# Kernel optimization log

Measured on AMD Instinct MI355X. Metric: run time of the kernel, lower is better.

The kernel has to match this reference:

```python
import jax, jax.numpy as jnp
import numpy as np

N = 50000      # nodes
E = 800000     # edges (avg in-degree 16, first N are self-loops)
H = 8          # heads
D = 16         # per-head dim (out_dim in the torch module)
IN = 128       # in_dim (= H*D)
SCALE = float(np.sqrt(D))


def setup_inputs() -> dict:
    key = jax.random.key(0)
    ks = jax.random.split(key, 8)
    query = jax.random.normal(ks[0], (N, IN), jnp.float32)
    key_x = jax.random.normal(ks[1], (N, IN), jnp.float32)
    value = jax.random.normal(ks[2], (N, IN), jnp.float32)
    # nn.Linear weights [out_features, in_features], no bias (use_bias=False)
    w_std = 1.0 / np.sqrt(IN)
    WQ = jax.random.normal(ks[3], (H * D, IN), jnp.float32) * w_std
    WK = jax.random.normal(ks[4], (H * D, IN), jnp.float32) * w_std
    WV = jax.random.normal(ks[5], (H * D, IN), jnp.float32) * w_std
    # edges: self-loops for every node (guarantees in-degree >= 1) + random edges
    loops = jnp.arange(N, dtype=jnp.int32)
    rsrc = jax.random.randint(ks[6], (E - N,), 0, N, jnp.int32)
    rdst = jax.random.randint(ks[7], (E - N,), 0, N, jnp.int32)
    edge_src = jnp.concatenate([loops, rsrc])
    edge_dst = jnp.concatenate([loops, rdst])
    return {"query": query, "key": key_x, "value": value,
            "WQ": WQ, "WK": WK, "WV": WV,
            "edge_src": edge_src, "edge_dst": edge_dst}


def reference(query, key, value, WQ, WK, WV, edge_src, edge_dst):
    n = query.shape[0]
    Qh = (query @ WQ.T).reshape(n, H, D)   # [N,H,D]
    Kh = (key @ WK.T).reshape(n, H, D)
    Vh = (value @ WV.T).reshape(n, H, D)
    # per-edge score: sum over head dim of K[src] * Q[dst]  (src_dot_dst)
    s = jnp.einsum('ehd,ehd->eh', Kh[edge_src], Qh[edge_dst])  # [E,H]
    # scaled_exp: exp(clamp(score / sqrt(D), -5, 5))
    a = jnp.exp(jnp.clip(s / SCALE, -5.0, 5.0))                # [E,H]
    # scatter-sum weighted V and normalizer z to destination nodes
    wV = jax.ops.segment_sum(a[:, :, None] * Vh[edge_src], edge_dst, num_segments=n)  # [N,H,D]
    z = jax.ops.segment_sum(a, edge_dst, num_segments=n)                               # [N,H]
    return wV / z[:, :, None]
```

## Files before the change

kernel.cpp:

```cpp
#include <hip/hip_runtime.h>

#define HD  128
#define CAP 64

typedef short bf16x8 __attribute__((ext_vector_type(8)));
typedef float f32x4  __attribute__((ext_vector_type(4)));

static __device__ __forceinline__ unsigned short f2bf_bits(float f) {
    union { float f; unsigned u; } x; x.f = f;
    unsigned r = x.u + 0x7FFF + ((x.u >> 16) & 1);
    return (unsigned short)(r >> 16);
}
static __device__ __forceinline__ float bf2f(unsigned short s) {
    union { unsigned u; float f; } x; x.u = ((unsigned)s) << 16;
    return x.f;
}

__global__ __launch_bounds__(256) void k_scatcvt(
    const int* __restrict__ esrc, const int* __restrict__ edst,
    int* __restrict__ cursor, int* __restrict__ csr, int E, int nsb,
    const float* __restrict__ wq, const float* __restrict__ wk,
    const float* __restrict__ wv, short* __restrict__ wb)
{
    int bid = blockIdx.x;
    if (bid < nsb) {
        int i = bid * 256 + threadIdx.x;
        if (i < E) {
            int d = edst[i];
            int p = atomicAdd(&cursor[d], 1);
            if (p < CAP) csr[d * CAP + p] = esrc[i];
        }
        return;
    }
    int t = (bid - nsb) * 256 + threadIdx.x;
    if (t >= 3 * 16384 / 4) return;
    int flat = t * 4;
    int m = flat >> 14;
    int off = flat & 16383;
    const float* W = (m == 0) ? wq : (m == 1) ? wk : wv;
    float4 v = *(const float4*)(W + off);
    short4 s;
    s.x = (short)f2bf_bits(v.x);
    s.y = (short)f2bf_bits(v.y);
    s.z = (short)f2bf_bits(v.z);
    s.w = (short)f2bf_bits(v.w);
    *(short4*)(wb + flat) = s;
}

__global__ __launch_bounds__(256) void k_proj(
    const float* __restrict__ q, const float* __restrict__ k, const float* __restrict__ v,
    const short* __restrict__ wb,
    float* __restrict__ qh, short* __restrict__ kvb,
    int n, int ntiles)
{
    int pid = blockIdx.x;
    int m = pid / ntiles;
    int tile = pid - m * ntiles;
    const float* X = (m == 0) ? q : (m == 1) ? k : v;
    const short* W = wb + m * 16384;

    int wave = threadIdx.x >> 6, lane = threadIdx.x & 63;
    int lm = lane & 15, lg = lane >> 4;
    const short* wp = W + lm * HD + lg * 8;

    int row0 = tile * 64 + wave * 16;
    int arow = row0 + lm; if (arow >= n) arow = n - 1;
    const float* xp = X + (size_t)arow * HD + lg * 8;

    bf16x8 a[4];
    #pragma unroll
    for (int kk = 0; kk < 4; kk++) {
        float4 p0 = *(const float4*)(xp + kk * 32);
        float4 p1 = *(const float4*)(xp + kk * 32 + 4);
        bf16x8 t;
        t[0] = (short)f2bf_bits(p0.x); t[1] = (short)f2bf_bits(p0.y);
        t[2] = (short)f2bf_bits(p0.z); t[3] = (short)f2bf_bits(p0.w);
        t[4] = (short)f2bf_bits(p1.x); t[5] = (short)f2bf_bits(p1.y);
        t[6] = (short)f2bf_bits(p1.z); t[7] = (short)f2bf_bits(p1.w);
        a[kk] = t;
    }

    f32x4 acc[8];
    #pragma unroll
    for (int nt = 0; nt < 8; nt++) { f32x4 z = {0.f, 0.f, 0.f, 0.f}; acc[nt] = z; }

    #pragma unroll
    for (int nt = 0; nt < 8; nt++) {
        #pragma unroll
        for (int kk = 0; kk < 4; kk++) {
            bf16x8 b = *(const bf16x8*)(wp + nt * 16 * HD + kk * 32);
            acc[nt] = __builtin_amdgcn_mfma_f32_16x16x32_bf16(a[kk], b, acc[nt], 0, 0, 0);
        }
    }

    if (m == 0) {
        #pragma unroll
        for (int nt = 0; nt < 8; nt++)
            #pragma unroll
            for (int i = 0; i < 4; i++) {
                int r = row0 + lg * 4 + i;
                if (r < n) qh[(size_t)r * HD + nt * 16 + lm] = acc[nt][i];
            }
    } else {
        short* base = kvb + ((m == 1) ? 0 : HD);
        #pragma unroll
        for (int nt = 0; nt < 8; nt++)
            #pragma unroll
            for (int i = 0; i < 4; i++) {
                int r = row0 + lg * 4 + i;
                if (r < n) base[(size_t)r * 256 + nt * 16 + lm] =
                    (short)f2bf_bits(acc[nt][i]);
            }
    }
}

__global__ __launch_bounds__(256) void k_gather(
    const float* __restrict__ qh, const short* __restrict__ kvb,
    const int* __restrict__ cursor, const int* __restrict__ csr,
    float* __restrict__ out, int n)
{
    int wave = threadIdx.x >> 6;
    int lane = threadIdx.x & 63;
    int v = blockIdx.x * 4 + wave;
    if (v >= n) return;
    int j = lane & 31;

    float4 qv = *(const float4*)&qh[(size_t)v * HD + 4 * j];
    int beg = v * CAP;
    int cnt = cursor[v]; if (cnt > CAP) cnt = CAP;
    int end = beg + cnt;

    float4 acc = {0.f, 0.f, 0.f, 0.f};
    float z = 0.f;

    int e = beg;
    for (; e + 3 < end; e += 4) {
        int u0 = csr[e];
        int u1 = csr[e + 1];
        int u2 = csr[e + 2];
        int u3 = csr[e + 3];
        ushort4 kv0 = *(const ushort4*)&kvb[(size_t)u0 * 256 + 4 * lane];
        ushort4 kv1 = *(const ushort4*)&kvb[(size_t)u1 * 256 + 4 * lane];
        ushort4 kv2 = *(const ushort4*)&kvb[(size_t)u2 * 256 + 4 * lane];
        ushort4 kv3 = *(const ushort4*)&kvb[(size_t)u3 * 256 + 4 * lane];
        float x00 = bf2f(kv0.x), x01 = bf2f(kv0.y), x02 = bf2f(kv0.z), x03 = bf2f(kv0.w);
        float x10 = bf2f(kv1.x), x11 = bf2f(kv1.y), x12 = bf2f(kv1.z), x13 = bf2f(kv1.w);
        float x20 = bf2f(kv2.x), x21 = bf2f(kv2.y), x22 = bf2f(kv2.z), x23 = bf2f(kv2.w);
        float x30 = bf2f(kv3.x), x31 = bf2f(kv3.y), x32 = bf2f(kv3.z), x33 = bf2f(kv3.w);
        float p0 = x00 * qv.x + x01 * qv.y + x02 * qv.z + x03 * qv.w;
        float p1 = x10 * qv.x + x11 * qv.y + x12 * qv.z + x13 * qv.w;
        float p2 = x20 * qv.x + x21 * qv.y + x22 * qv.z + x23 * qv.w;
        float p3 = x30 * qv.x + x31 * qv.y + x32 * qv.z + x33 * qv.w;
        p0 += __shfl_xor(p0, 1); p1 += __shfl_xor(p1, 1);
        p2 += __shfl_xor(p2, 1); p3 += __shfl_xor(p3, 1);
        p0 += __shfl_xor(p0, 2); p1 += __shfl_xor(p1, 2);
        p2 += __shfl_xor(p2, 2); p3 += __shfl_xor(p3, 2);
        float a0 = __expf(fminf(fmaxf(p0 * 0.25f, -5.f), 5.f));
        float a1 = __expf(fminf(fmaxf(p1 * 0.25f, -5.f), 5.f));
        float a2 = __expf(fminf(fmaxf(p2 * 0.25f, -5.f), 5.f));
        float a3 = __expf(fminf(fmaxf(p3 * 0.25f, -5.f), 5.f));
        float av0 = __shfl_xor(a0, 32);
        float av1 = __shfl_xor(a1, 32);
        float av2 = __shfl_xor(a2, 32);
        float av3 = __shfl_xor(a3, 32);
        z += (a0 + a1) + (a2 + a3);
        acc.x += av0 * x00 + av1 * x10 + av2 * x20 + av3 * x30;
        acc.y += av0 * x01 + av1 * x11 + av2 * x21 + av3 * x31;
        acc.z += av0 * x02 + av1 * x12 + av2 * x22 + av3 * x32;
        acc.w += av0 * x03 + av1 * x13 + av2 * x23 + av3 * x33;
    }
    for (; e < end; ++e) {
        int u = csr[e];
        ushort4 kv = *(const ushort4*)&kvb[(size_t)u * 256 + 4 * lane];
        float x0 = bf2f(kv.x), x1 = bf2f(kv.y), x2 = bf2f(kv.z), x3 = bf2f(kv.w);
        float p = x0 * qv.x + x1 * qv.y + x2 * qv.z + x3 * qv.w;
        p += __shfl_xor(p, 1);
        p += __shfl_xor(p, 2);
        float a = __expf(fminf(fmaxf(p * 0.25f, -5.f), 5.f));
        float av = __shfl_xor(a, 32);
        z += a;
        acc.x += av * x0; acc.y += av * x1; acc.z += av * x2; acc.w += av * x3;
    }

    float zz = __shfl_xor(z, 32);
    if (lane >= 32) {
        float inv = 1.f / zz;
        float4 o = { acc.x * inv, acc.y * inv, acc.z * inv, acc.w * inv };
        *(float4*)&out[(size_t)v * HD + 4 * j] = o;
    }
}

extern "C" void kernel_launch(void* const* d_in, const int* in_sizes, int n_in,
                              void* d_out, int out_size, void* d_ws, size_t ws_size,
                              hipStream_t stream)
{
    const float* query = (const float*)d_in[0];
    const float* key   = (const float*)d_in[1];
    const float* value = (const float*)d_in[2];
    const float* WQ    = (const float*)d_in[3];
    const float* WK    = (const float*)d_in[4];
    const float* WV    = (const float*)d_in[5];
    const int*   esrc  = (const int*)d_in[6];
    const int*   edst  = (const int*)d_in[7];
    int n = in_sizes[0] / HD;
    int E = in_sizes[6];

    char* ws = (char*)d_ws;
    size_t off = 0;
    auto carve = [&](size_t bytes) -> void* {
        void* p = ws + off;
        off += (bytes + 255) & ~size_t(255);
        return p;
    };
    float* qh     = (float*)carve((size_t)n * HD * 4);
    short* kvb    = (short*)carve((size_t)n * 256 * 2);
    short* wb     = (short*)carve((size_t)3 * 16384 * 2);
    int*   cursor = (int*)carve((size_t)n * 4);
    int*   csr    = (int*)carve((size_t)n * CAP * 4);
    (void)ws_size;

    hipMemsetAsync(cursor, 0, (size_t)n * 4, stream);

    int nsb = (E + 255) / 256;
    k_scatcvt<<<nsb + 48, 256, 0, stream>>>(esrc, edst, cursor, csr, E, nsb,
                                            WQ, WK, WV, wb);

    int ntiles = (n + 63) / 64;
    k_proj<<<3 * ntiles, 256, 0, stream>>>(query, key, value, wb, qh, kvb, n, ntiles);

    k_gather<<<(n + 3) / 4, 256, 0, stream>>>(qh, kvb, cursor, csr,
                                              (float*)d_out, n);
}
```

Measured before the change: 168.2 us.

## Fuse edge scatter with projection, two row tiles per block, kernel zeroing

```diff
diff --git a/kernel.cpp b/kernel.cpp
--- a/kernel.cpp
+++ b/kernel.cpp
@@ -16,11 +16,36 @@
     return x.f;
 }
 
-__global__ __launch_bounds__(256) void k_scatcvt(
+__global__ __launch_bounds__(256) void k_pre(
+    const float* __restrict__ wq, const float* __restrict__ wk,
+    const float* __restrict__ wv, short* __restrict__ wb,
+    int* __restrict__ cursor, int n)
+{
+    int t = blockIdx.x * blockDim.x + threadIdx.x;
+    int nthr = gridDim.x * blockDim.x;
+    for (int i = t; i < 3 * 16384 / 4; i += nthr) {
+        int flat = i * 4;
+        int m = flat >> 14;
+        int off = flat & 16383;
+        const float* W = (m == 0) ? wq : (m == 1) ? wk : wv;
+        float4 v = *(const float4*)(W + off);
+        short4 s;
+        s.x = (short)f2bf_bits(v.x);
+        s.y = (short)f2bf_bits(v.y);
+        s.z = (short)f2bf_bits(v.z);
+        s.w = (short)f2bf_bits(v.w);
+        *(short4*)(wb + flat) = s;
+    }
+    for (int i = t; i < n; i += nthr) cursor[i] = 0;
+}
+
+__global__ __launch_bounds__(256) void k_spro(
     const int* __restrict__ esrc, const int* __restrict__ edst,
     int* __restrict__ cursor, int* __restrict__ csr, int E, int nsb,
-    const float* __restrict__ wq, const float* __restrict__ wk,
-    const float* __restrict__ wv, short* __restrict__ wb)
+    const float* __restrict__ q, const float* __restrict__ k, const float* __restrict__ v,
+    const short* __restrict__ wb,
+    float* __restrict__ qh, short* __restrict__ kvb,
+    int n, int npairs)
 {
     int bid = blockIdx.x;
     if (bid < nsb) {
@@ -32,30 +57,9 @@
         }
         return;
     }
-    int t = (bid - nsb) * 256 + threadIdx.x;
-    if (t >= 3 * 16384 / 4) return;
-    int flat = t * 4;
-    int m = flat >> 14;
-    int off = flat & 16383;
-    const float* W = (m == 0) ? wq : (m == 1) ? wk : wv;
-    float4 v = *(const float4*)(W + off);
-    short4 s;
-    s.x = (short)f2bf_bits(v.x);
-    s.y = (short)f2bf_bits(v.y);
-    s.z = (short)f2bf_bits(v.z);
-    s.w = (short)f2bf_bits(v.w);
-    *(short4*)(wb + flat) = s;
-}
-
-__global__ __launch_bounds__(256) void k_proj(
-    const float* __restrict__ q, const float* __restrict__ k, const float* __restrict__ v,
-    const short* __restrict__ wb,
-    float* __restrict__ qh, short* __restrict__ kvb,
-    int n, int ntiles)
-{
-    int pid = blockIdx.x;
-    int m = pid / ntiles;
-    int tile = pid - m * ntiles;
+    int pid = bid - nsb;
+    int m = pid / npairs;
+    int pr = pid - m * npairs;
     const float* X = (m == 0) ? q : (m == 1) ? k : v;
     const short* W = wb + m * 16384;
 
@@ -63,33 +67,51 @@
     int lm = lane & 15, lg = lane >> 4;
     const short* wp = W + lm * HD + lg * 8;
 
-    int row0 = tile * 64 + wave * 16;
-    int arow = row0 + lm; if (arow >= n) arow = n - 1;
-    const float* xp = X + (size_t)arow * HD + lg * 8;
-
-    bf16x8 a[4];
+    int rowA = pr * 128 + wave * 16;
+    int rowB = rowA + 64;
+    int arA = rowA + lm; if (arA >= n) arA = n - 1;
+    int arB = rowB + lm; if (arB >= n) arB = n - 1;
+    const float* xpA = X + (size_t)arA * HD + lg * 8;
+    const float* xpB = X + (size_t)arB * HD + lg * 8;
+
+    float4 pA[8], pB[8];
     #pragma unroll
     for (int kk = 0; kk < 4; kk++) {
-        float4 p0 = *(const float4*)(xp + kk * 32);
-        float4 p1 = *(const float4*)(xp + kk * 32 + 4);
-        bf16x8 t;
-        t[0] = (short)f2bf_bits(p0.x); t[1] = (short)f2bf_bits(p0.y);
-        t[2] = (short)f2bf_bits(p0.z); t[3] = (short)f2bf_bits(p0.w);
-        t[4] = (short)f2bf_bits(p1.x); t[5] = (short)f2bf_bits(p1.y);
-        t[6] = (short)f2bf_bits(p1.z); t[7] = (short)f2bf_bits(p1.w);
-        a[kk] = t;
-    }
-
-    f32x4 acc[8];
-    #pragma unroll
-    for (int nt = 0; nt < 8; nt++) { f32x4 z = {0.f, 0.f, 0.f, 0.f}; acc[nt] = z; }
+        pA[2 * kk]     = *(const float4*)(xpA + kk * 32);
+        pA[2 * kk + 1] = *(const float4*)(xpA + kk * 32 + 4);
+        pB[2 * kk]     = *(const float4*)(xpB + kk * 32);
+        pB[2 * kk + 1] = *(const float4*)(xpB + kk * 32 + 4);
+    }
+    bf16x8 a0[4], a1[4];
+    #pragma unroll
+    for (int kk = 0; kk < 4; kk++) {
+        bf16x8 t0, t1;
+        t0[0] = (short)f2bf_bits(pA[2*kk].x);   t0[1] = (short)f2bf_bits(pA[2*kk].y);
+        t0[2] = (short)f2bf_bits(pA[2*kk].z);   t0[3] = (short)f2bf_bits(pA[2*kk].w);
+        t0[4] = (short)f2bf_bits(pA[2*kk+1].x); t0[5] = (short)f2bf_bits(pA[2*kk+1].y);
+        t0[6] = (short)f2bf_bits(pA[2*kk+1].z); t0[7] = (short)f2bf_bits(pA[2*kk+1].w);
+        a0[kk] = t0;
+        t1[0] = (short)f2bf_bits(pB[2*kk].x);   t1[1] = (short)f2bf_bits(pB[2*kk].y);
+        t1[2] = (short)f2bf_bits(pB[2*kk].z);   t1[3] = (short)f2bf_bits(pB[2*kk].w);
+        t1[4] = (short)f2bf_bits(pB[2*kk+1].x); t1[5] = (short)f2bf_bits(pB[2*kk+1].y);
+        t1[6] = (short)f2bf_bits(pB[2*kk+1].z); t1[7] = (short)f2bf_bits(pB[2*kk+1].w);
+        a1[kk] = t1;
+    }
+
+    f32x4 acc0[8], acc1[8];
+    #pragma unroll
+    for (int nt = 0; nt < 8; nt++) {
+        f32x4 z = {0.f, 0.f, 0.f, 0.f};
+        acc0[nt] = z; acc1[nt] = z;
+    }
 
     #pragma unroll
     for (int nt = 0; nt < 8; nt++) {
         #pragma unroll
         for (int kk = 0; kk < 4; kk++) {
             bf16x8 b = *(const bf16x8*)(wp + nt * 16 * HD + kk * 32);
-            acc[nt] = __builtin_amdgcn_mfma_f32_16x16x32_bf16(a[kk], b, acc[nt], 0, 0, 0);
+            acc0[nt] = __builtin_amdgcn_mfma_f32_16x16x32_bf16(a0[kk], b, acc0[nt], 0, 0, 0);
+            acc1[nt] = __builtin_amdgcn_mfma_f32_16x16x32_bf16(a1[kk], b, acc1[nt], 0, 0, 0);
         }
     }
 
@@ -98,8 +120,10 @@
         for (int nt = 0; nt < 8; nt++)
             #pragma unroll
             for (int i = 0; i < 4; i++) {
-                int r = row0 + lg * 4 + i;
-                if (r < n) qh[(size_t)r * HD + nt * 16 + lm] = acc[nt][i];
+                int rA = rowA + lg * 4 + i;
+                int rB = rowB + lg * 4 + i;
+                if (rA < n) qh[(size_t)rA * HD + nt * 16 + lm] = acc0[nt][i];
+                if (rB < n) qh[(size_t)rB * HD + nt * 16 + lm] = acc1[nt][i];
             }
     } else {
         short* base = kvb + ((m == 1) ? 0 : HD);
@@ -107,9 +131,12 @@
         for (int nt = 0; nt < 8; nt++)
             #pragma unroll
             for (int i = 0; i < 4; i++) {
-                int r = row0 + lg * 4 + i;
-                if (r < n) base[(size_t)r * 256 + nt * 16 + lm] =
-                    (short)f2bf_bits(acc[nt][i]);
+                int rA = rowA + lg * 4 + i;
+                int rB = rowB + lg * 4 + i;
+                if (rA < n) base[(size_t)rA * 256 + nt * 16 + lm] =
+                    (short)f2bf_bits(acc0[nt][i]);
+                if (rB < n) base[(size_t)rB * 256 + nt * 16 + lm] =
+                    (short)f2bf_bits(acc1[nt][i]);
             }
     }
 }
@@ -219,14 +246,14 @@
     int*   csr    = (int*)carve((size_t)n * CAP * 4);
     (void)ws_size;
 
-    hipMemsetAsync(cursor, 0, (size_t)n * 4, stream);
+    k_pre<<<64, 256, 0, stream>>>(WQ, WK, WV, wb, cursor, n);
 
     int nsb = (E + 255) / 256;
-    k_scatcvt<<<nsb + 48, 256, 0, stream>>>(esrc, edst, cursor, csr, E, nsb,
-                                            WQ, WK, WV, wb);
-
     int ntiles = (n + 63) / 64;
-    k_proj<<<3 * ntiles, 256, 0, stream>>>(query, key, value, wb, qh, kvb, n, ntiles);
+    int npairs = (ntiles + 1) / 2;
+    k_spro<<<nsb + 3 * npairs, 256, 0, stream>>>(esrc, edst, cursor, csr, E, nsb,
+                                                 query, key, value, wb, qh, kvb,
+                                                 n, npairs);
 
     k_gather<<<(n + 3) / 4, 256, 0, stream>>>(qh, kvb, cursor, csr,
                                               (float*)d_out, n);
```

Result: no change. 165.8 us (-1.4%).

## Stage projection outputs through swizzled LDS and deepen gather unroll to eight

Applied to the files above, without the earlier changes.

```diff
diff --git a/kernel.cpp b/kernel.cpp
--- a/kernel.cpp
+++ b/kernel.cpp
@@ -16,35 +16,39 @@
     return x.f;
 }
 
-__global__ __launch_bounds__(256) void k_scatcvt(
+__global__ __launch_bounds__(256) void k_pre(
+    const float* __restrict__ wq, const float* __restrict__ wk,
+    const float* __restrict__ wv, short* __restrict__ wb,
+    int* __restrict__ cursor, int n)
+{
+    int t = blockIdx.x * blockDim.x + threadIdx.x;
+    int nthr = gridDim.x * blockDim.x;
+    for (int i = t; i < 3 * 16384 / 4; i += nthr) {
+        int flat = i * 4;
+        int m = flat >> 14;
+        int off = flat & 16383;
+        const float* W = (m == 0) ? wq : (m == 1) ? wk : wv;
+        float4 v = *(const float4*)(W + off);
+        short4 s;
+        s.x = (short)f2bf_bits(v.x);
+        s.y = (short)f2bf_bits(v.y);
+        s.z = (short)f2bf_bits(v.z);
+        s.w = (short)f2bf_bits(v.w);
+        *(short4*)(wb + flat) = s;
+    }
+    for (int i = t; i < n; i += nthr) cursor[i] = 0;
+}
+
+__global__ __launch_bounds__(256) void k_scat(
     const int* __restrict__ esrc, const int* __restrict__ edst,
-    int* __restrict__ cursor, int* __restrict__ csr, int E, int nsb,
-    const float* __restrict__ wq, const float* __restrict__ wk,
-    const float* __restrict__ wv, short* __restrict__ wb)
-{
-    int bid = blockIdx.x;
-    if (bid < nsb) {
-        int i = bid * 256 + threadIdx.x;
-        if (i < E) {
-            int d = edst[i];
-            int p = atomicAdd(&cursor[d], 1);
-            if (p < CAP) csr[d * CAP + p] = esrc[i];
-        }
-        return;
-    }
-    int t = (bid - nsb) * 256 + threadIdx.x;
-    if (t >= 3 * 16384 / 4) return;
-    int flat = t * 4;
-    int m = flat >> 14;
-    int off = flat & 16383;
-    const float* W = (m == 0) ? wq : (m == 1) ? wk : wv;
-    float4 v = *(const float4*)(W + off);
-    short4 s;
-    s.x = (short)f2bf_bits(v.x);
-    s.y = (short)f2bf_bits(v.y);
-    s.z = (short)f2bf_bits(v.z);
-    s.w = (short)f2bf_bits(v.w);
-    *(short4*)(wb + flat) = s;
+    int* __restrict__ cursor, int* __restrict__ csr, int E)
+{
+    int i = blockIdx.x * 256 + threadIdx.x;
+    if (i < E) {
+        int d = edst[i];
+        int p = atomicAdd(&cursor[d], 1);
+        if (p < CAP) csr[d * CAP + p] = esrc[i];
+    }
 }
 
 __global__ __launch_bounds__(256) void k_proj(
@@ -53,6 +57,7 @@
     float* __restrict__ qh, short* __restrict__ kvb,
     int n, int ntiles)
 {
+    __shared__ float smem[64 * 128];
     int pid = blockIdx.x;
     int m = pid / ntiles;
     int tile = pid - m * ntiles;
@@ -63,8 +68,9 @@
     int lm = lane & 15, lg = lane >> 4;
     const short* wp = W + lm * HD + lg * 8;
 
-    int row0 = tile * 64 + wave * 16;
-    int arow = row0 + lm; if (arow >= n) arow = n - 1;
+    int row0 = tile * 64;
+    int rw = row0 + wave * 16;
+    int arow = rw + lm; if (arow >= n) arow = n - 1;
     const float* xp = X + (size_t)arow * HD + lg * 8;
 
     bf16x8 a[4];
@@ -98,19 +104,49 @@
         for (int nt = 0; nt < 8; nt++)
             #pragma unroll
             for (int i = 0; i < 4; i++) {
-                int r = row0 + lg * 4 + i;
-                if (r < n) qh[(size_t)r * HD + nt * 16 + lm] = acc[nt][i];
-            }
+                int rl = wave * 16 + lg * 4 + i;
+                smem[rl * 128 + ((nt ^ (rl & 7)) * 16 + lm)] = acc[nt][i];
+            }
+        __syncthreads();
+        int t = threadIdx.x;
+        #pragma unroll
+        for (int p = 0; p < 4; p++) {
+            int flat = p * 256 + t;
+            int r = flat >> 4;
+            int c8 = (flat & 15) * 8;
+            int g = c8 >> 4, rem = c8 & 15;
+            const float* sp = &smem[r * 128 + ((g ^ (r & 7)) * 16 + rem)];
+            int rg = row0 + r;
+            if (rg < n) {
+                *(float4*)&qh[(size_t)rg * HD + c8]     = *(const float4*)sp;
+                *(float4*)&qh[(size_t)rg * HD + c8 + 4] = *(const float4*)(sp + 4);
+            }
+        }
     } else {
-        short* base = kvb + ((m == 1) ? 0 : HD);
+        short* sb = (short*)smem;
         #pragma unroll
         for (int nt = 0; nt < 8; nt++)
             #pragma unroll
             for (int i = 0; i < 4; i++) {
-                int r = row0 + lg * 4 + i;
-                if (r < n) base[(size_t)r * 256 + nt * 16 + lm] =
-                    (short)f2bf_bits(acc[nt][i]);
-            }
+                int rl = wave * 16 + lg * 4 + i;
+                sb[rl * 128 + ((nt ^ (rl & 7)) * 16 + lm)] = (short)f2bf_bits(acc[nt][i]);
+            }
+        __syncthreads();
+        int t = threadIdx.x;
+        int coff = (m == 1) ? 0 : HD;
+        #pragma unroll
+        for (int p = 0; p < 4; p++) {
+            int flat = p * 256 + t;
+            int r = flat >> 4;
+            int c8 = (flat & 15) * 8;
+            int g = c8 >> 4, rem = c8 & 15;
+            const short* sp = &sb[r * 128 + ((g ^ (r & 7)) * 16 + rem)];
+            int rg = row0 + r;
+            if (rg < n) {
+                *(short4*)&kvb[(size_t)rg * 256 + coff + c8]     = *(const short4*)sp;
+                *(short4*)&kvb[(size_t)rg * 256 + coff + c8 + 4] = *(const short4*)(sp + 4);
+            }
+        }
     }
 }
 
@@ -134,40 +170,60 @@
     float z = 0.f;
 
     int e = beg;
+    for (; e + 7 < end; e += 8) {
+        int u[8];
+        #pragma unroll
+        for (int q8 = 0; q8 < 8; q8++) u[q8] = csr[e + q8];
+        ushort4 kvx[8];
+        #pragma unroll
+        for (int q8 = 0; q8 < 8; q8++)
+            kvx[q8] = *(const ushort4*)&kvb[(size_t)u[q8] * 256 + 4 * lane];
+        float x0[8], x1[8], x2[8], x3[8], p[8];
+        #pragma unroll
+        for (int q8 = 0; q8 < 8; q8++) {
+            x0[q8] = bf2f(kvx[q8].x); x1[q8] = bf2f(kvx[q8].y);
+            x2[q8] = bf2f(kvx[q8].z); x3[q8] = bf2f(kvx[q8].w);
+            p[q8] = x0[q8] * qv.x + x1[q8] * qv.y + x2[q8] * qv.z + x3[q8] * qv.w;
+        }
+        #pragma unroll
+        for (int q8 = 0; q8 < 8; q8++) p[q8] += __shfl_xor(p[q8], 1);
+        #pragma unroll
+        for (int q8 = 0; q8 < 8; q8++) p[q8] += __shfl_xor(p[q8], 2);
+        float a[8], av[8];
+        #pragma unroll
+        for (int q8 = 0; q8 < 8; q8++)
+            a[q8] = __expf(fminf(fmaxf(p[q8] * 0.25f, -5.f), 5.f));
+        #pragma unroll
+        for (int q8 = 0; q8 < 8; q8++) av[q8] = __shfl_xor(a[q8], 32);
+        #pragma unroll
+        for (int q8 = 0; q8 < 8; q8++) {
+            z += a[q8];
+            acc.x += av[q8] * x0[q8];
+            acc.y += av[q8] * x1[q8];
+            acc.z += av[q8] * x2[q8];
+            acc.w += av[q8] * x3[q8];
+        }
+    }
     for (; e + 3 < end; e += 4) {
-        int u0 = csr[e];
-        int u1 = csr[e + 1];
-        int u2 = csr[e + 2];
-        int u3 = csr[e + 3];
-        ushort4 kv0 = *(const ushort4*)&kvb[(size_t)u0 * 256 + 4 * lane];
-        ushort4 kv1 = *(const ushort4*)&kvb[(size_t)u1 * 256 + 4 * lane];
-        ushort4 kv2 = *(const ushort4*)&kvb[(size_t)u2 * 256 + 4 * lane];
-        ushort4 kv3 = *(const ushort4*)&kvb[(size_t)u3 * 256 + 4 * lane];
-        float x00 = bf2f(kv0.x), x01 = bf2f(kv0.y), x02 = bf2f(kv0.z), x03 = bf2f(kv0.w);
-        float x10 = bf2f(kv1.x), x11 = bf2f(kv1.y), x12 = bf2f(kv1.z), x13 = bf2f(kv1.w);
-        float x20 = bf2f(kv2.x), x21 = bf2f(kv2.y), x22 = bf2f(kv2.z), x23 = bf2f(kv2.w);
-        float x30 = bf2f(kv3.x), x31 = bf2f(kv3.y), x32 = bf2f(kv3.z), x33 = bf2f(kv3.w);
-        float p0 = x00 * qv.x + x01 * qv.y + x02 * qv.z + x03 * qv.w;
-        float p1 = x10 * qv.x + x11 * qv.y + x12 * qv.z + x13 * qv.w;
-        float p2 = x20 * qv.x + x21 * qv.y + x22 * qv.z + x23 * qv.w;
-        float p3 = x30 * qv.x + x31 * qv.y + x32 * qv.z + x33 * qv.w;
-        p0 += __shfl_xor(p0, 1); p1 += __shfl_xor(p1, 1);
-        p2 += __shfl_xor(p2, 1); p3 += __shfl_xor(p3, 1);
-        p0 += __shfl_xor(p0, 2); p1 += __shfl_xor(p1, 2);
-        p2 += __shfl_xor(p2, 2); p3 += __shfl_xor(p3, 2);
-        float a0 = __expf(fminf(fmaxf(p0 * 0.25f, -5.f), 5.f));
-        float a1 = __expf(fminf(fmaxf(p1 * 0.25f, -5.f), 5.f));
-        float a2 = __expf(fminf(fmaxf(p2 * 0.25f, -5.f), 5.f));
-        float a3 = __expf(fminf(fmaxf(p3 * 0.25f, -5.f), 5.f));
-        float av0 = __shfl_xor(a0, 32);
-        float av1 = __shfl_xor(a1, 32);
-        float av2 = __shfl_xor(a2, 32);
-        float av3 = __shfl_xor(a3, 32);
-        z += (a0 + a1) + (a2 + a3);
-        acc.x += av0 * x00 + av1 * x10 + av2 * x20 + av3 * x30;
-        acc.y += av0 * x01 + av1 * x11 + av2 * x21 + av3 * x31;
-        acc.z += av0 * x02 + av1 * x12 + av2 * x22 + av3 * x32;
-        acc.w += av0 * x03 + av1 * x13 + av2 * x23 + av3 * x33;
+        int u[4];
+        #pragma unroll
+        for (int q4 = 0; q4 < 4; q4++) u[q4] = csr[e + q4];
+        ushort4 kvx[4];
+        #pragma unroll
+        for (int q4 = 0; q4 < 4; q4++)
+            kvx[q4] = *(const ushort4*)&kvb[(size_t)u[q4] * 256 + 4 * lane];
+        #pragma unroll
+        for (int q4 = 0; q4 < 4; q4++) {
+            float x0 = bf2f(kvx[q4].x), x1 = bf2f(kvx[q4].y);
+            float x2 = bf2f(kvx[q4].z), x3 = bf2f(kvx[q4].w);
+            float p = x0 * qv.x + x1 * qv.y + x2 * qv.z + x3 * qv.w;
+            p += __shfl_xor(p, 1);
+            p += __shfl_xor(p, 2);
+            float a = __expf(fminf(fmaxf(p * 0.25f, -5.f), 5.f));
+            float av = __shfl_xor(a, 32);
+            z += a;
+            acc.x += av * x0; acc.y += av * x1; acc.z += av * x2; acc.w += av * x3;
+        }
     }
     for (; e < end; ++e) {
         int u = csr[e];
@@ -219,11 +275,9 @@
     int*   csr    = (int*)carve((size_t)n * CAP * 4);
     (void)ws_size;
 
-    hipMemsetAsync(cursor, 0, (size_t)n * 4, stream);
-
-    int nsb = (E + 255) / 256;
-    k_scatcvt<<<nsb + 48, 256, 0, stream>>>(esrc, edst, cursor, csr, E, nsb,
-                                            WQ, WK, WV, wb);
+    k_pre<<<64, 256, 0, stream>>>(WQ, WK, WV, wb, cursor, n);
+
+    k_scat<<<(E + 255) / 256, 256, 0, stream>>>(esrc, edst, cursor, csr, E);
 
     int ntiles = (n + 63) / 64;
     k_proj<<<3 * ntiles, 256, 0, stream>>>(query, key, value, wb, qh, kvb, n, ntiles);
```

Result: slower. 179.0 us (+6.4%).

## Stage bf16 weights in swizzled LDS with persistent projection blocks

Applied to the files above, without the earlier changes.

```diff
diff --git a/kernel.cpp b/kernel.cpp
--- a/kernel.cpp
+++ b/kernel.cpp
@@ -16,35 +16,39 @@
     return x.f;
 }
 
-__global__ __launch_bounds__(256) void k_scatcvt(
+__global__ __launch_bounds__(256) void k_pre(
+    const float* __restrict__ wq, const float* __restrict__ wk,
+    const float* __restrict__ wv, short* __restrict__ wb,
+    int* __restrict__ cursor, int n)
+{
+    int t = blockIdx.x * blockDim.x + threadIdx.x;
+    int nthr = gridDim.x * blockDim.x;
+    for (int i = t; i < 3 * 16384 / 4; i += nthr) {
+        int flat = i * 4;
+        int m = flat >> 14;
+        int off = flat & 16383;
+        const float* W = (m == 0) ? wq : (m == 1) ? wk : wv;
+        float4 v = *(const float4*)(W + off);
+        short4 s;
+        s.x = (short)f2bf_bits(v.x);
+        s.y = (short)f2bf_bits(v.y);
+        s.z = (short)f2bf_bits(v.z);
+        s.w = (short)f2bf_bits(v.w);
+        *(short4*)(wb + flat) = s;
+    }
+    for (int i = t; i < n; i += nthr) cursor[i] = 0;
+}
+
+__global__ __launch_bounds__(256) void k_scat(
     const int* __restrict__ esrc, const int* __restrict__ edst,
-    int* __restrict__ cursor, int* __restrict__ csr, int E, int nsb,
-    const float* __restrict__ wq, const float* __restrict__ wk,
-    const float* __restrict__ wv, short* __restrict__ wb)
-{
-    int bid = blockIdx.x;
-    if (bid < nsb) {
-        int i = bid * 256 + threadIdx.x;
-        if (i < E) {
-            int d = edst[i];
-            int p = atomicAdd(&cursor[d], 1);
-            if (p < CAP) csr[d * CAP + p] = esrc[i];
-        }
-        return;
-    }
-    int t = (bid - nsb) * 256 + threadIdx.x;
-    if (t >= 3 * 16384 / 4) return;
-    int flat = t * 4;
-    int m = flat >> 14;
-    int off = flat & 16383;
-    const float* W = (m == 0) ? wq : (m == 1) ? wk : wv;
-    float4 v = *(const float4*)(W + off);
-    short4 s;
-    s.x = (short)f2bf_bits(v.x);
-    s.y = (short)f2bf_bits(v.y);
-    s.z = (short)f2bf_bits(v.z);
-    s.w = (short)f2bf_bits(v.w);
-    *(short4*)(wb + flat) = s;
+    int* __restrict__ cursor, int* __restrict__ csr, int E)
+{
+    int i = blockIdx.x * 256 + threadIdx.x;
+    if (i < E) {
+        int d = edst[i];
+        int p = atomicAdd(&cursor[d], 1);
+        if (p < CAP) csr[d * CAP + p] = esrc[i];
+    }
 }
 
 __global__ __launch_bounds__(256) void k_proj(
@@ -53,64 +57,79 @@
     float* __restrict__ qh, short* __restrict__ kvb,
     int n, int ntiles)
 {
-    int pid = blockIdx.x;
-    int m = pid / ntiles;
-    int tile = pid - m * ntiles;
+    __shared__ short wlds[16384];
+    int bid = blockIdx.x;
+    int m = bid % 3;
+    int t0 = bid / 3;
     const float* X = (m == 0) ? q : (m == 1) ? k : v;
     const short* W = wb + m * 16384;
 
-    int wave = threadIdx.x >> 6, lane = threadIdx.x & 63;
+    int tid = threadIdx.x;
+    for (int i = tid; i < 2048; i += 256) {
+        int row = i >> 4, g = i & 15;
+        *(bf16x8*)&wlds[row * 128 + ((g ^ (row & 15)) * 8)] =
+            *(const bf16x8*)&W[row * 128 + g * 8];
+    }
+    __syncthreads();
+
+    int wave = tid >> 6, lane = tid & 63;
     int lm = lane & 15, lg = lane >> 4;
-    const short* wp = W + lm * HD + lg * 8;
-
-    int row0 = tile * 64 + wave * 16;
-    int arow = row0 + lm; if (arow >= n) arow = n - 1;
-    const float* xp = X + (size_t)arow * HD + lg * 8;
-
-    bf16x8 a[4];
-    #pragma unroll
-    for (int kk = 0; kk < 4; kk++) {
-        float4 p0 = *(const float4*)(xp + kk * 32);
-        float4 p1 = *(const float4*)(xp + kk * 32 + 4);
-        bf16x8 t;
-        t[0] = (short)f2bf_bits(p0.x); t[1] = (short)f2bf_bits(p0.y);
-        t[2] = (short)f2bf_bits(p0.z); t[3] = (short)f2bf_bits(p0.w);
-        t[4] = (short)f2bf_bits(p1.x); t[5] = (short)f2bf_bits(p1.y);
-        t[6] = (short)f2bf_bits(p1.z); t[7] = (short)f2bf_bits(p1.w);
-        a[kk] = t;
-    }
-
-    f32x4 acc[8];
-    #pragma unroll
-    for (int nt = 0; nt < 8; nt++) { f32x4 z = {0.f, 0.f, 0.f, 0.f}; acc[nt] = z; }
-
-    #pragma unroll
-    for (int nt = 0; nt < 8; nt++) {
+
+    for (int tile = t0; tile < ntiles; tile += 256) {
+        int row0 = tile * 64 + wave * 16;
+        int arow = row0 + lm; if (arow >= n) arow = n - 1;
+        const float* xp = X + (size_t)arow * HD + lg * 8;
+
+        float4 p0[4], p1[4];
         #pragma unroll
         for (int kk = 0; kk < 4; kk++) {
-            bf16x8 b = *(const bf16x8*)(wp + nt * 16 * HD + kk * 32);
-            acc[nt] = __builtin_amdgcn_mfma_f32_16x16x32_bf16(a[kk], b, acc[nt], 0, 0, 0);
-        }
-    }
-
-    if (m == 0) {
-        #pragma unroll
-        for (int nt = 0; nt < 8; nt++)
+            p0[kk] = *(const float4*)(xp + kk * 32);
+            p1[kk] = *(const float4*)(xp + kk * 32 + 4);
+        }
+        bf16x8 a[4];
+        #pragma unroll
+        for (int kk = 0; kk < 4; kk++) {
+            bf16x8 t;
+            t[0] = (short)f2bf_bits(p0[kk].x); t[1] = (short)f2bf_bits(p0[kk].y);
+            t[2] = (short)f2bf_bits(p0[kk].z); t[3] = (short)f2bf_bits(p0[kk].w);
+            t[4] = (short)f2bf_bits(p1[kk].x); t[5] = (short)f2bf_bits(p1[kk].y);
+            t[6] = (short)f2bf_bits(p1[kk].z); t[7] = (short)f2bf_bits(p1[kk].w);
+            a[kk] = t;
+        }
+
+        f32x4 acc[8];
+        #pragma unroll
+        for (int nt = 0; nt < 8; nt++) { f32x4 z = {0.f, 0.f, 0.f, 0.f}; acc[nt] = z; }
+
+        #pragma unroll
+        for (int nt = 0; nt < 8; nt++) {
             #pragma unroll
-            for (int i = 0; i < 4; i++) {
-                int r = row0 + lg * 4 + i;
-                if (r < n) qh[(size_t)r * HD + nt * 16 + lm] = acc[nt][i];
+            for (int kk = 0; kk < 4; kk++) {
+                bf16x8 b = *(const bf16x8*)&wlds[(nt * 16 + lm) * 128 +
+                                                 (((lg + 4 * kk) ^ lm) * 8)];
+                acc[nt] = __builtin_amdgcn_mfma_f32_16x16x32_bf16(a[kk], b, acc[nt], 0, 0, 0);
             }
-    } else {
-        short* base = kvb + ((m == 1) ? 0 : HD);
-        #pragma unroll
-        for (int nt = 0; nt < 8; nt++)
+        }
+
+        if (m == 0) {
             #pragma unroll
-            for (int i = 0; i < 4; i++) {
-                int r = row0 + lg * 4 + i;
-                if (r < n) base[(size_t)r * 256 + nt * 16 + lm] =
-                    (short)f2bf_bits(acc[nt][i]);
-            }
+            for (int nt = 0; nt < 8; nt++)
+                #pragma unroll
+                for (int i = 0; i < 4; i++) {
+                    int r = row0 + lg * 4 + i;
+                    if (r < n) qh[(size_t)r * HD + nt * 16 + lm] = acc[nt][i];
+                }
+        } else {
+            short* base = kvb + ((m == 1) ? 0 : HD);
+            #pragma unroll
+            for (int nt = 0; nt < 8; nt++)
+                #pragma unroll
+                for (int i = 0; i < 4; i++) {
+                    int r = row0 + lg * 4 + i;
+                    if (r < n) base[(size_t)r * 256 + nt * 16 + lm] =
+                        (short)f2bf_bits(acc[nt][i]);
+                }
+        }
     }
 }
 
@@ -219,14 +238,12 @@
     int*   csr    = (int*)carve((size_t)n * CAP * 4);
     (void)ws_size;
 
-    hipMemsetAsync(cursor, 0, (size_t)n * 4, stream);
-
-    int nsb = (E + 255) / 256;
-    k_scatcvt<<<nsb + 48, 256, 0, stream>>>(esrc, edst, cursor, csr, E, nsb,
-                                            WQ, WK, WV, wb);
+    k_pre<<<64, 256, 0, stream>>>(WQ, WK, WV, wb, cursor, n);
+
+    k_scat<<<(E + 255) / 256, 256, 0, stream>>>(esrc, edst, cursor, csr, E);
 
     int ntiles = (n + 63) / 64;
-    k_proj<<<3 * ntiles, 256, 0, stream>>>(query, key, value, wb, qh, kvb, n, ntiles);
+    k_proj<<<768, 256, 0, stream>>>(query, key, value, wb, qh, kvb, n, ntiles);
 
     k_gather<<<(n + 3) / 4, 256, 0, stream>>>(qh, kvb, cursor, csr,
                                               (float*)d_out, n);
```

After: 140.1 us. -16.7%, faster.
